# Kernel optimization log

Hardware: AMD Instinct MI355X
Metric: run time of the kernel (lower is better)

The kernel has to match this reference:

```python
import jax, jax.numpy as jnp
import numpy as np

N_TOKENS = 8192
DIM = 2048
HIDDEN = 1408
N_EXPERTS = 8
CAP = N_TOKENS // N_EXPERTS  # balanced routing: tokens per expert


def setup_inputs() -> dict:
    key = jax.random.key(0)
    kx, k1, k2, k3 = jax.random.split(key, 4)
    x = jax.random.normal(kx, (N_TOKENS, DIM), dtype=jnp.float32)
    # trunc_normal(std=0.02)-scale init approximated by scaled normal
    w1 = jax.random.normal(k1, (N_EXPERTS, HIDDEN, DIM), dtype=jnp.float32) * 0.02
    w2 = jax.random.normal(k2, (N_EXPERTS, DIM, HIDDEN), dtype=jnp.float32) * 0.02
    w3 = jax.random.normal(k3, (N_EXPERTS, HIDDEN, DIM), dtype=jnp.float32) * 0.02
    # tokens already permuted expert-contiguously; balanced load here
    num_tokens_per_expert = jnp.full((N_EXPERTS,), CAP, dtype=jnp.int32)
    return {"x": x, "num_tokens_per_expert": num_tokens_per_expert, "w1": w1, "w2": w2, "w3": w3}


def _grouped_swiglu(x, num_tokens_per_expert, w1, w2, w3):
    # x: [N, D]; w1/w3: [E, H, D]; w2: [E, D, H]. Tokens are contiguous per expert.
    E, H, D = w1.shape
    N = x.shape[0]
    cap = N // E  # fixed per-expert tile (>= max tokens of any expert here)
    offsets = jnp.cumsum(num_tokens_per_expert)
    starts = offsets - num_tokens_per_expert  # [E]

    def one_expert(w1e, w3e, w2e, start):
        # slice this expert's token tile: [cap, D]
        xe = jax.lax.dynamic_slice(x, (start, 0), (cap, D))
        h = jax.nn.silu(xe @ w1e.T) * (xe @ w3e.T)  # [cap, H] fused SwiGLU gate-up
        return h @ w2e.T  # [cap, D] down projection

    outs = jax.vmap(one_expert)(w1, w3, w2, starts)  # [E, cap, D] ragged grouped GEMM
    # mask slots beyond each expert's token count, scatter tiles back to [N, D]
    valid = jnp.arange(cap)[None, :] < num_tokens_per_expert[:, None]  # [E, cap]
    outs = jnp.where(valid[..., None], outs, jnp.zeros((), x.dtype))
    pos = jnp.clip(starts[:, None] + jnp.arange(cap)[None, :], 0, N - 1)
    out = jnp.zeros((N, D), x.dtype).at[pos.reshape(-1)].add(outs.reshape(-1, D))
    return out


def reference(x, num_tokens_per_expert, w1, w2, w3):
    return _grouped_swiglu(x, num_tokens_per_expert, w1, w2, w3)
```

## Files before the change

kernel.cpp:

```cpp
#include <hip/hip_runtime.h>
#include <hip/hip_bf16.h>

#define NT   8192
#define DD   2048
#define HH   1408
#define NE   8
#define CAPT 1024

typedef __bf16 bf16x8 __attribute__((ext_vector_type(8)));
typedef float  f32x4  __attribute__((ext_vector_type(4)));
typedef unsigned short us8 __attribute__((ext_vector_type(8)));

__device__ __forceinline__ unsigned short f2bf(float f) {
  union { float f; unsigned u; } v; v.f = f;
  unsigned r = v.u + 0x7fffu + ((v.u >> 16) & 1u);
  return (unsigned short)(r >> 16);
}

__device__ __forceinline__ void load_lds16(const void* g, void* l) {
  __builtin_amdgcn_global_load_lds(
      (const __attribute__((address_space(1))) unsigned int*)g,
      (__attribute__((address_space(3))) unsigned int*)l, 16, 0, 0);
}

__global__ __launch_bounds__(256) void cvt_bf16_kernel(
    const float* __restrict__ in, unsigned short* __restrict__ out) {
  size_t i = ((size_t)blockIdx.x * 256 + threadIdx.x) * 8;
  const float4* p = reinterpret_cast<const float4*>(in + i);
  float4 a = p[0], b = p[1];
  us8 o;
  o[0] = f2bf(a.x); o[1] = f2bf(a.y); o[2] = f2bf(a.z); o[3] = f2bf(a.w);
  o[4] = f2bf(b.x); o[5] = f2bf(b.y); o[6] = f2bf(b.z); o[7] = f2bf(b.w);
  *reinterpret_cast<us8*>(out + i) = o;
}

__global__ __launch_bounds__(256) void gateup_gemm(
    const unsigned short* __restrict__ xb,
    const unsigned short* __restrict__ w1b,
    const unsigned short* __restrict__ w3b,
    const int* __restrict__ counts,
    unsigned short* __restrict__ h)
{
  __shared__ __align__(16) unsigned short As[128 * 32];
  __shared__ __align__(16) unsigned short B1s[64 * 32];
  __shared__ __align__(16) unsigned short B3s[64 * 32];

  const int e  = blockIdx.z;
  const int m0 = blockIdx.y * 128;
  const int n0 = blockIdx.x * 64;

  int start = 0;
  for (int i = 0; i < e; ++i) start += counts[i];

  const int tid  = threadIdx.x;
  const int lane = tid & 63;
  const int wid  = tid >> 6;
  const int lrow = lane >> 2;
  const int lcol = (lane & 3) * 8;

  const unsigned short* ga  = xb  + (size_t)(start + m0 + wid * 32 + lrow) * DD + lcol;
  const unsigned short* gb1 = w1b + ((size_t)e * HH + n0 + wid * 16 + lrow) * DD + lcol;
  const unsigned short* gb3 = w3b + ((size_t)e * HH + n0 + wid * 16 + lrow) * DD + lcol;

  unsigned short* lA0 = &As [(wid * 32) * 32      + lane * 8];
  unsigned short* lA1 = &As [(wid * 32 + 16) * 32 + lane * 8];
  unsigned short* lB1 = &B1s[(wid * 16) * 32      + lane * 8];
  unsigned short* lB3 = &B3s[(wid * 16) * 32      + lane * 8];

  const int fm  = lane & 15;
  const int fko = (lane >> 4) * 8;
  const int wm  = (wid >> 1) * 64;
  const int wn  = (wid & 1) * 32;

  f32x4 acc[2][4][2] = {};

  for (int k0 = 0; k0 < DD; k0 += 32) {
    load_lds16(ga,           lA0);
    load_lds16(ga + 16 * DD, lA1);
    load_lds16(gb1,          lB1);
    load_lds16(gb3,          lB3);
    ga += 32; gb1 += 32; gb3 += 32;
    __builtin_amdgcn_s_waitcnt(0x3f70);
    __syncthreads();

    bf16x8 af[4];
#pragma unroll
    for (int i = 0; i < 4; ++i)
      af[i] = *reinterpret_cast<const bf16x8*>(&As[(wm + i * 16 + fm) * 32 + fko]);
#pragma unroll
    for (int j = 0; j < 2; ++j) {
      bf16x8 b1 = *reinterpret_cast<const bf16x8*>(&B1s[(wn + j * 16 + fm) * 32 + fko]);
      bf16x8 b3 = *reinterpret_cast<const bf16x8*>(&B3s[(wn + j * 16 + fm) * 32 + fko]);
#pragma unroll
      for (int i = 0; i < 4; ++i) {
        acc[0][i][j] = __builtin_amdgcn_mfma_f32_16x16x32_bf16(af[i], b1, acc[0][i][j], 0, 0, 0);
        acc[1][i][j] = __builtin_amdgcn_mfma_f32_16x16x32_bf16(af[i], b3, acc[1][i][j], 0, 0, 0);
      }
    }
    __syncthreads();
  }

  const int r0 = (lane >> 4) * 4;
#pragma unroll
  for (int i = 0; i < 4; ++i)
#pragma unroll
    for (int j = 0; j < 2; ++j)
#pragma unroll
      for (int r = 0; r < 4; ++r) {
        int row = m0 + wm + i * 16 + r0 + r;
        int col = n0 + wn + j * 16 + fm;
        float gv = acc[0][i][j][r];
        float uv = acc[1][i][j][r];
        float sv = (gv / (1.0f + __expf(-gv))) * uv;
        h[(size_t)(start + row) * HH + col] = f2bf(sv);
      }
}

__global__ __launch_bounds__(256) void down_gemm(
    const unsigned short* __restrict__ hb,
    const unsigned short* __restrict__ w2b,
    const int* __restrict__ counts,
    float* __restrict__ out)
{
  __shared__ __align__(16) unsigned short Hs[128 * 32];
  __shared__ __align__(16) unsigned short Ws[128 * 32];

  const int e  = blockIdx.z;
  const int m0 = blockIdx.y * 128;
  const int n0 = blockIdx.x * 128;

  int start = 0;
  for (int i = 0; i < e; ++i) start += counts[i];

  const int tid  = threadIdx.x;
  const int lane = tid & 63;
  const int wid  = tid >> 6;
  const int lrow = lane >> 2;
  const int lcol = (lane & 3) * 8;

  const unsigned short* ga = hb  + (size_t)(start + m0 + wid * 32 + lrow) * HH + lcol;
  const unsigned short* gb = w2b + ((size_t)e * DD + n0 + wid * 32 + lrow) * HH + lcol;

  unsigned short* lH0 = &Hs[(wid * 32) * 32      + lane * 8];
  unsigned short* lH1 = &Hs[(wid * 32 + 16) * 32 + lane * 8];
  unsigned short* lW0 = &Ws[(wid * 32) * 32      + lane * 8];
  unsigned short* lW1 = &Ws[(wid * 32 + 16) * 32 + lane * 8];

  const int fm  = lane & 15;
  const int fko = (lane >> 4) * 8;
  const int wm  = (wid >> 1) * 64;
  const int wn  = (wid & 1) * 64;

  f32x4 acc[4][4] = {};

  for (int k0 = 0; k0 < HH; k0 += 32) {
    load_lds16(ga,           lH0);
    load_lds16(ga + 16 * HH, lH1);
    load_lds16(gb,           lW0);
    load_lds16(gb + 16 * HH, lW1);
    ga += 32; gb += 32;
    __builtin_amdgcn_s_waitcnt(0x3f70);
    __syncthreads();

    bf16x8 af[4];
#pragma unroll
    for (int i = 0; i < 4; ++i)
      af[i] = *reinterpret_cast<const bf16x8*>(&Hs[(wm + i * 16 + fm) * 32 + fko]);
#pragma unroll
    for (int j = 0; j < 4; ++j) {
      bf16x8 bf_ = *reinterpret_cast<const bf16x8*>(&Ws[(wn + j * 16 + fm) * 32 + fko]);
#pragma unroll
      for (int i = 0; i < 4; ++i)
        acc[i][j] = __builtin_amdgcn_mfma_f32_16x16x32_bf16(af[i], bf_, acc[i][j], 0, 0, 0);
    }
    __syncthreads();
  }

  const int r0 = (lane >> 4) * 4;
#pragma unroll
  for (int i = 0; i < 4; ++i)
#pragma unroll
    for (int j = 0; j < 4; ++j)
#pragma unroll
      for (int r = 0; r < 4; ++r) {
        int row = m0 + wm + i * 16 + r0 + r;
        int col = n0 + wn + j * 16 + fm;
        out[(size_t)(start + row) * DD + col] = acc[i][j][r];
      }
}

extern "C" void kernel_launch(void* const* d_in, const int* in_sizes, int n_in,
                              void* d_out, int out_size, void* d_ws, size_t ws_size,
                              hipStream_t stream) {
  const float* x  = (const float*)d_in[0];
  const int*   cn = (const int*)d_in[1];
  const float* w1 = (const float*)d_in[2];
  const float* w2 = (const float*)d_in[3];
  const float* w3 = (const float*)d_in[4];
  float* out = (float*)d_out;

  char* ws = (char*)d_ws;
  unsigned short* xb  = (unsigned short*)(ws + 0);
  unsigned short* w1b = (unsigned short*)(ws + 33554432);
  unsigned short* w3b = (unsigned short*)(ws + 79691776);
  unsigned short* hb  = (unsigned short*)(ws + 125829120);
  unsigned short* w2b = (unsigned short*)(ws + 0);

  cvt_bf16_kernel<<<(NT * DD) / 2048, 256, 0, stream>>>(x, xb);
  cvt_bf16_kernel<<<(NE * HH * DD) / 2048, 256, 0, stream>>>(w1, w1b);
  cvt_bf16_kernel<<<(NE * HH * DD) / 2048, 256, 0, stream>>>(w3, w3b);

  dim3 g1(HH / 64, CAPT / 128, NE);
  gateup_gemm<<<g1, 256, 0, stream>>>(xb, w1b, w3b, cn, hb);

  cvt_bf16_kernel<<<(NE * DD * HH) / 2048, 256, 0, stream>>>(w2, w2b);

  dim3 g2(DD / 128, CAPT / 128, NE);
  down_gemm<<<g2, 256, 0, stream>>>(hb, w2b, cn, out);
}
```

Baseline: 533.4 us.

## Rewrite grouped GEMMs with 256-tile, double-buffered LDS pipeline and swizzled layout

Both GEMM kernels move to 512-thread blocks with 256x128 (gate-up) and 256x256 (down) tiles and a 64-wide K step. Global-to-LDS loads are double-buffered and interleaved between four MFMA phases, using explicit vmcnt waits, barriers and s_setprio. LDS uses an XOR swizzle to avoid bank conflicts, and block indices are remapped so concurrently running blocks share an expert. The aim is to raise data reuse and hide memory latency, in exchange for 128KB of dynamic LDS per block, more registers and hand-tuned synchronisation that is fragile.

```diff
diff --git a/kernel.cpp b/kernel.cpp
--- a/kernel.cpp
+++ b/kernel.cpp
@@ -1,5 +1,4 @@
 #include <hip/hip_runtime.h>
-#include <hip/hip_bf16.h>
 
 #define NT   8192
 #define DD   2048
@@ -11,6 +10,8 @@
 typedef float  f32x4  __attribute__((ext_vector_type(4)));
 typedef unsigned short us8 __attribute__((ext_vector_type(8)));
 
+#define MFMA16(a, b, c) __builtin_amdgcn_mfma_f32_16x16x32_bf16((a), (b), (c), 0, 0, 0)
+
 __device__ __forceinline__ unsigned short f2bf(float f) {
   union { float f; unsigned u; } v; v.f = f;
   unsigned r = v.u + 0x7fffu + ((v.u >> 16) & 1u);
@@ -21,6 +22,18 @@
   __builtin_amdgcn_global_load_lds(
       (const __attribute__((address_space(1))) unsigned int*)g,
       (__attribute__((address_space(3))) unsigned int*)l, 16, 0, 0);
+}
+
+#define BAR() do { asm volatile("" ::: "memory"); \
+                   __builtin_amdgcn_s_barrier();  \
+                   asm volatile("" ::: "memory"); } while (0)
+#define VMCNT6() asm volatile("s_waitcnt vmcnt(6)" ::: "memory")
+#define VMCNT0() asm volatile("s_waitcnt vmcnt(0)" ::: "memory")
+
+__device__ __forceinline__ void stage2(const unsigned short* src, unsigned short* dst,
+                                       int dchunk, int ld) {
+  load_lds16(src,                  dst + dchunk);
+  load_lds16(src + (size_t)8 * ld, dst + dchunk + 512);
 }
 
 __global__ __launch_bounds__(256) void cvt_bf16_kernel(
@@ -34,159 +47,305 @@
   *reinterpret_cast<us8*>(out + i) = o;
 }
 
-__global__ __launch_bounds__(256) void gateup_gemm(
+__global__ __launch_bounds__(512, 2) void gateup_gemm(
     const unsigned short* __restrict__ xb,
     const unsigned short* __restrict__ w1b,
     const unsigned short* __restrict__ w3b,
     const int* __restrict__ counts,
     unsigned short* __restrict__ h)
 {
-  __shared__ __align__(16) unsigned short As[128 * 32];
-  __shared__ __align__(16) unsigned short B1s[64 * 32];
-  __shared__ __align__(16) unsigned short B3s[64 * 32];
-
-  const int e  = blockIdx.z;
-  const int m0 = blockIdx.y * 128;
-  const int n0 = blockIdx.x * 64;
+  extern __shared__ unsigned short lds[];
+
+  int lin = blockIdx.x + 11 * (blockIdx.y + 4 * blockIdx.z);
+  lin = (lin & 7) * 44 + (lin >> 3);
+  const int e   = lin / 44;
+  const int rem = lin - e * 44;
+  const int m0  = (rem / 11) * 256;
+  const int n0  = (rem - (rem / 11) * 11) * 128;
 
   int start = 0;
   for (int i = 0; i < e; ++i) start += counts[i];
 
   const int tid  = threadIdx.x;
   const int lane = tid & 63;
-  const int wid  = tid >> 6;
-  const int lrow = lane >> 2;
-  const int lcol = (lane & 3) * 8;
-
-  const unsigned short* ga  = xb  + (size_t)(start + m0 + wid * 32 + lrow) * DD + lcol;
-  const unsigned short* gb1 = w1b + ((size_t)e * HH + n0 + wid * 16 + lrow) * DD + lcol;
-  const unsigned short* gb3 = w3b + ((size_t)e * HH + n0 + wid * 16 + lrow) * DD + lcol;
-
-  unsigned short* lA0 = &As [(wid * 32) * 32      + lane * 8];
-  unsigned short* lA1 = &As [(wid * 32 + 16) * 32 + lane * 8];
-  unsigned short* lB1 = &B1s[(wid * 16) * 32      + lane * 8];
-  unsigned short* lB3 = &B3s[(wid * 16) * 32      + lane * 8];
-
-  const int fm  = lane & 15;
-  const int fko = (lane >> 4) * 8;
-  const int wm  = (wid >> 1) * 64;
-  const int wn  = (wid & 1) * 32;
-
-  f32x4 acc[2][4][2] = {};
-
-  for (int k0 = 0; k0 < DD; k0 += 32) {
-    load_lds16(ga,           lA0);
-    load_lds16(ga + 16 * DD, lA1);
-    load_lds16(gb1,          lB1);
-    load_lds16(gb3,          lB3);
-    ga += 32; gb1 += 32; gb3 += 32;
-    __builtin_amdgcn_s_waitcnt(0x3f70);
-    __syncthreads();
-
-    bf16x8 af[4];
-#pragma unroll
-    for (int i = 0; i < 4; ++i)
-      af[i] = *reinterpret_cast<const bf16x8*>(&As[(wm + i * 16 + fm) * 32 + fko]);
-#pragma unroll
-    for (int j = 0; j < 2; ++j) {
-      bf16x8 b1 = *reinterpret_cast<const bf16x8*>(&B1s[(wn + j * 16 + fm) * 32 + fko]);
-      bf16x8 b3 = *reinterpret_cast<const bf16x8*>(&B3s[(wn + j * 16 + fm) * 32 + fko]);
-#pragma unroll
-      for (int i = 0; i < 4; ++i) {
-        acc[0][i][j] = __builtin_amdgcn_mfma_f32_16x16x32_bf16(af[i], b1, acc[0][i][j], 0, 0, 0);
-        acc[1][i][j] = __builtin_amdgcn_mfma_f32_16x16x32_bf16(af[i], b3, acc[1][i][j], 0, 0, 0);
-      }
-    }
-    __syncthreads();
+  const int w    = tid >> 6;
+  const int wr   = w >> 2;
+  const int wc   = w & 3;
+  const int fm   = lane & 15;
+  const int l4   = lane >> 4;
+  const int s0   = (l4 ^ (fm & 7)) << 3;
+  const int s1   = s0 ^ 32;
+  const int srcR = w * 16 + (lane >> 3);
+  const int srcC = ((lane & 7) ^ (lane >> 3)) << 3;
+  const int dchunk = w * 1024 + lane * 8;
+
+  const unsigned short* gA  = xb  + (size_t)(start + m0 + srcR) * DD + srcC;
+  const unsigned short* gB1 = w1b + ((size_t)e * HH + n0 + srcR) * DD + srcC;
+  const unsigned short* gB3 = w3b + ((size_t)e * HH + n0 + srcR) * DD + srcC;
+
+  unsigned short* ldsA = lds;
+  unsigned short* ldsB = lds + 32768;
+
+  stage2(gA,                       ldsA,                 dchunk, DD);
+  stage2(gA + (size_t)128 * DD,    ldsA + 8192,          dchunk, DD);
+  stage2(gB1,                      ldsB,                 dchunk, DD);
+  stage2(gB3,                      ldsB + 8192,          dchunk, DD);
+  stage2(gB1 + 64,                 ldsB + 16384,         dchunk, DD);
+  stage2(gA + 64,                  ldsA + 16384,         dchunk, DD);
+  stage2(gA + (size_t)128 * DD + 64, ldsA + 16384 + 8192, dchunk, DD);
+  VMCNT6();
+  BAR();
+
+  f32x4 accG[8][2] = {};
+  f32x4 accU[8][2] = {};
+  const int NTL = DD / 64;
+
+  for (int t = 0; t < NTL; ++t) {
+    const int buf  = (t & 1) << 14;
+    const int obuf = buf ^ 16384;
+    const unsigned short* At = ldsA + buf + wr * 8192 + fm * 64;
+    const unsigned short* Bg = ldsB + buf + (wc * 32 + fm) * 64;
+    const unsigned short* Bu = Bg + 8192;
+    bf16x8 a0[4][2], a1[4][2], bg[2][2], bu[2][2];
+
+#pragma unroll
+    for (int mi = 0; mi < 4; ++mi) {
+      a0[mi][0] = *(const bf16x8*)(At + mi * 1024 + s0);
+      a0[mi][1] = *(const bf16x8*)(At + mi * 1024 + s1);
+    }
+#pragma unroll
+    for (int nj = 0; nj < 2; ++nj) {
+      bg[nj][0] = *(const bf16x8*)(Bg + nj * 1024 + s0);
+      bg[nj][1] = *(const bf16x8*)(Bg + nj * 1024 + s1);
+    }
+    if (t + 1 < NTL) stage2(gB3 + (t + 1) * 64, ldsB + obuf + 8192, dchunk, DD);
+    BAR();
+    __builtin_amdgcn_s_setprio(1);
+#pragma unroll
+    for (int mi = 0; mi < 4; ++mi)
+#pragma unroll
+      for (int nj = 0; nj < 2; ++nj) {
+        accG[mi][nj] = MFMA16(a0[mi][0], bg[nj][0], accG[mi][nj]);
+        accG[mi][nj] = MFMA16(a0[mi][1], bg[nj][1], accG[mi][nj]);
+      }
+    __builtin_amdgcn_s_setprio(0);
+    BAR();
+
+#pragma unroll
+    for (int mi = 0; mi < 4; ++mi) {
+      a1[mi][0] = *(const bf16x8*)(At + (mi + 4) * 1024 + s0);
+      a1[mi][1] = *(const bf16x8*)(At + (mi + 4) * 1024 + s1);
+    }
+    if (t + 2 < NTL) stage2(gB1 + (t + 2) * 64, ldsB + buf, dchunk, DD);
+    BAR();
+    __builtin_amdgcn_s_setprio(1);
+#pragma unroll
+    for (int mi = 0; mi < 4; ++mi)
+#pragma unroll
+      for (int nj = 0; nj < 2; ++nj) {
+        accG[mi + 4][nj] = MFMA16(a1[mi][0], bg[nj][0], accG[mi + 4][nj]);
+        accG[mi + 4][nj] = MFMA16(a1[mi][1], bg[nj][1], accG[mi + 4][nj]);
+      }
+    __builtin_amdgcn_s_setprio(0);
+    BAR();
+
+#pragma unroll
+    for (int nj = 0; nj < 2; ++nj) {
+      bu[nj][0] = *(const bf16x8*)(Bu + nj * 1024 + s0);
+      bu[nj][1] = *(const bf16x8*)(Bu + nj * 1024 + s1);
+    }
+    if (t + 2 < NTL) stage2(gA + (t + 2) * 64, ldsA + buf, dchunk, DD);
+    BAR();
+    __builtin_amdgcn_s_setprio(1);
+#pragma unroll
+    for (int mi = 0; mi < 4; ++mi)
+#pragma unroll
+      for (int nj = 0; nj < 2; ++nj) {
+        accU[mi][nj] = MFMA16(a0[mi][0], bu[nj][0], accU[mi][nj]);
+        accU[mi][nj] = MFMA16(a0[mi][1], bu[nj][1], accU[mi][nj]);
+      }
+    __builtin_amdgcn_s_setprio(0);
+    BAR();
+
+    if (t + 2 < NTL) {
+      stage2(gA + (size_t)128 * DD + (t + 2) * 64, ldsA + buf + 8192, dchunk, DD);
+      VMCNT6();
+    } else if (t + 1 < NTL) {
+      VMCNT0();
+    }
+    BAR();
+    __builtin_amdgcn_s_setprio(1);
+#pragma unroll
+    for (int mi = 0; mi < 4; ++mi)
+#pragma unroll
+      for (int nj = 0; nj < 2; ++nj) {
+        accU[mi + 4][nj] = MFMA16(a1[mi][0], bu[nj][0], accU[mi + 4][nj]);
+        accU[mi + 4][nj] = MFMA16(a1[mi][1], bu[nj][1], accU[mi + 4][nj]);
+      }
+    __builtin_amdgcn_s_setprio(0);
+    BAR();
   }
 
-  const int r0 = (lane >> 4) * 4;
-#pragma unroll
-  for (int i = 0; i < 4; ++i)
-#pragma unroll
-    for (int j = 0; j < 2; ++j)
+  const int r0 = l4 * 4;
+  const size_t hbase = (size_t)(start + m0 + wr * 128) * HH + n0 + wc * 32 + fm;
+#pragma unroll
+  for (int mi = 0; mi < 8; ++mi)
+#pragma unroll
+    for (int nj = 0; nj < 2; ++nj)
 #pragma unroll
       for (int r = 0; r < 4; ++r) {
-        int row = m0 + wm + i * 16 + r0 + r;
-        int col = n0 + wn + j * 16 + fm;
-        float gv = acc[0][i][j][r];
-        float uv = acc[1][i][j][r];
+        float gv = accG[mi][nj][r];
+        float uv = accU[mi][nj][r];
         float sv = (gv / (1.0f + __expf(-gv))) * uv;
-        h[(size_t)(start + row) * HH + col] = f2bf(sv);
-      }
-}
-
-__global__ __launch_bounds__(256) void down_gemm(
+        h[hbase + (size_t)(mi * 16 + r0 + r) * HH + nj * 16] = f2bf(sv);
+      }
+}
+
+__global__ __launch_bounds__(512, 2) void down_gemm(
     const unsigned short* __restrict__ hb,
     const unsigned short* __restrict__ w2b,
     const int* __restrict__ counts,
     float* __restrict__ out)
 {
-  __shared__ __align__(16) unsigned short Hs[128 * 32];
-  __shared__ __align__(16) unsigned short Ws[128 * 32];
-
-  const int e  = blockIdx.z;
-  const int m0 = blockIdx.y * 128;
-  const int n0 = blockIdx.x * 128;
+  extern __shared__ unsigned short lds[];
+
+  int lin = blockIdx.x + 8 * (blockIdx.y + 4 * blockIdx.z);
+  lin = (lin & 7) * 32 + (lin >> 3);
+  const int e   = lin >> 5;
+  const int rem = lin & 31;
+  const int m0  = (rem >> 3) * 256;
+  const int n0  = (rem & 7) * 256;
 
   int start = 0;
   for (int i = 0; i < e; ++i) start += counts[i];
 
   const int tid  = threadIdx.x;
   const int lane = tid & 63;
-  const int wid  = tid >> 6;
-  const int lrow = lane >> 2;
-  const int lcol = (lane & 3) * 8;
-
-  const unsigned short* ga = hb  + (size_t)(start + m0 + wid * 32 + lrow) * HH + lcol;
-  const unsigned short* gb = w2b + ((size_t)e * DD + n0 + wid * 32 + lrow) * HH + lcol;
-
-  unsigned short* lH0 = &Hs[(wid * 32) * 32      + lane * 8];
-  unsigned short* lH1 = &Hs[(wid * 32 + 16) * 32 + lane * 8];
-  unsigned short* lW0 = &Ws[(wid * 32) * 32      + lane * 8];
-  unsigned short* lW1 = &Ws[(wid * 32 + 16) * 32 + lane * 8];
-
-  const int fm  = lane & 15;
-  const int fko = (lane >> 4) * 8;
-  const int wm  = (wid >> 1) * 64;
-  const int wn  = (wid & 1) * 64;
-
-  f32x4 acc[4][4] = {};
-
-  for (int k0 = 0; k0 < HH; k0 += 32) {
-    load_lds16(ga,           lH0);
-    load_lds16(ga + 16 * HH, lH1);
-    load_lds16(gb,           lW0);
-    load_lds16(gb + 16 * HH, lW1);
-    ga += 32; gb += 32;
-    __builtin_amdgcn_s_waitcnt(0x3f70);
-    __syncthreads();
-
-    bf16x8 af[4];
-#pragma unroll
-    for (int i = 0; i < 4; ++i)
-      af[i] = *reinterpret_cast<const bf16x8*>(&Hs[(wm + i * 16 + fm) * 32 + fko]);
-#pragma unroll
-    for (int j = 0; j < 4; ++j) {
-      bf16x8 bf_ = *reinterpret_cast<const bf16x8*>(&Ws[(wn + j * 16 + fm) * 32 + fko]);
-#pragma unroll
-      for (int i = 0; i < 4; ++i)
-        acc[i][j] = __builtin_amdgcn_mfma_f32_16x16x32_bf16(af[i], bf_, acc[i][j], 0, 0, 0);
-    }
-    __syncthreads();
+  const int w    = tid >> 6;
+  const int wr   = w >> 2;
+  const int wc   = w & 3;
+  const int fm   = lane & 15;
+  const int l4   = lane >> 4;
+  const int s0   = (l4 ^ (fm & 7)) << 3;
+  const int s1   = s0 ^ 32;
+  const int srcR = w * 16 + (lane >> 3);
+  const int srcC = ((lane & 7) ^ (lane >> 3)) << 3;
+  const int dchunk = w * 1024 + lane * 8;
+
+  const unsigned short* gA = hb  + (size_t)(start + m0 + srcR) * HH + srcC;
+  const unsigned short* gB = w2b + ((size_t)e * DD + n0 + srcR) * HH + srcC;
+
+  unsigned short* ldsA = lds;
+  unsigned short* ldsB = lds + 32768;
+
+  stage2(gA,                       ldsA,                 dchunk, HH);
+  stage2(gA + (size_t)128 * HH,    ldsA + 8192,          dchunk, HH);
+  stage2(gB,                       ldsB,                 dchunk, HH);
+  stage2(gB + (size_t)128 * HH,    ldsB + 8192,          dchunk, HH);
+  stage2(gA + 64,                  ldsA + 16384,         dchunk, HH);
+  stage2(gA + (size_t)128 * HH + 64, ldsA + 16384 + 8192, dchunk, HH);
+  stage2(gB + 64,                  ldsB + 16384,         dchunk, HH);
+  VMCNT6();
+  BAR();
+
+  f32x4 acc[8][4] = {};
+  const int NTL = HH / 64;
+
+  for (int t = 0; t < NTL; ++t) {
+    const int buf  = (t & 1) << 14;
+    const int obuf = buf ^ 16384;
+    const unsigned short* At = ldsA + buf + wr * 8192 + fm * 64;
+    const unsigned short* Bt = ldsB + buf + (wc >> 1) * 8192 + ((wc & 1) * 64 + fm) * 64;
+    bf16x8 a0[4][2], a1[4][2], b0[2][2], b1[2][2];
+
+#pragma unroll
+    for (int mi = 0; mi < 4; ++mi) {
+      a0[mi][0] = *(const bf16x8*)(At + mi * 1024 + s0);
+      a0[mi][1] = *(const bf16x8*)(At + mi * 1024 + s1);
+    }
+#pragma unroll
+    for (int nj = 0; nj < 2; ++nj) {
+      b0[nj][0] = *(const bf16x8*)(Bt + nj * 1024 + s0);
+      b0[nj][1] = *(const bf16x8*)(Bt + nj * 1024 + s1);
+    }
+    if (t + 1 < NTL)
+      stage2(gB + (size_t)128 * HH + (t + 1) * 64, ldsB + obuf + 8192, dchunk, HH);
+    BAR();
+    __builtin_amdgcn_s_setprio(1);
+#pragma unroll
+    for (int mi = 0; mi < 4; ++mi)
+#pragma unroll
+      for (int nj = 0; nj < 2; ++nj) {
+        acc[mi][nj] = MFMA16(a0[mi][0], b0[nj][0], acc[mi][nj]);
+        acc[mi][nj] = MFMA16(a0[mi][1], b0[nj][1], acc[mi][nj]);
+      }
+    __builtin_amdgcn_s_setprio(0);
+    BAR();
+
+#pragma unroll
+    for (int mi = 0; mi < 4; ++mi) {
+      a1[mi][0] = *(const bf16x8*)(At + (mi + 4) * 1024 + s0);
+      a1[mi][1] = *(const bf16x8*)(At + (mi + 4) * 1024 + s1);
+    }
+    BAR();
+    __builtin_amdgcn_s_setprio(1);
+#pragma unroll
+    for (int mi = 0; mi < 4; ++mi)
+#pragma unroll
+      for (int nj = 0; nj < 2; ++nj) {
+        acc[mi + 4][nj] = MFMA16(a1[mi][0], b0[nj][0], acc[mi + 4][nj]);
+        acc[mi + 4][nj] = MFMA16(a1[mi][1], b0[nj][1], acc[mi + 4][nj]);
+      }
+    __builtin_amdgcn_s_setprio(0);
+    BAR();
+
+#pragma unroll
+    for (int nj = 0; nj < 2; ++nj) {
+      b1[nj][0] = *(const bf16x8*)(Bt + (nj + 2) * 1024 + s0);
+      b1[nj][1] = *(const bf16x8*)(Bt + (nj + 2) * 1024 + s1);
+    }
+    if (t + 2 < NTL) stage2(gA + (t + 2) * 64, ldsA + buf, dchunk, HH);
+    BAR();
+    __builtin_amdgcn_s_setprio(1);
+#pragma unroll
+    for (int mi = 0; mi < 4; ++mi)
+#pragma unroll
+      for (int nj = 0; nj < 2; ++nj) {
+        acc[mi][nj + 2] = MFMA16(a0[mi][0], b1[nj][0], acc[mi][nj + 2]);
+        acc[mi][nj + 2] = MFMA16(a0[mi][1], b1[nj][1], acc[mi][nj + 2]);
+      }
+    __builtin_amdgcn_s_setprio(0);
+    BAR();
+
+    if (t + 2 < NTL) {
+      stage2(gA + (size_t)128 * HH + (t + 2) * 64, ldsA + buf + 8192, dchunk, HH);
+      stage2(gB + (t + 2) * 64,                    ldsB + buf,        dchunk, HH);
+      VMCNT6();
+    } else if (t + 1 < NTL) {
+      VMCNT0();
+    }
+    BAR();
+    __builtin_amdgcn_s_setprio(1);
+#pragma unroll
+    for (int mi = 0; mi < 4; ++mi)
+#pragma unroll
+      for (int nj = 0; nj < 2; ++nj) {
+        acc[mi + 4][nj + 2] = MFMA16(a1[mi][0], b1[nj][0], acc[mi + 4][nj + 2]);
+        acc[mi + 4][nj + 2] = MFMA16(a1[mi][1], b1[nj][1], acc[mi + 4][nj + 2]);
+      }
+    __builtin_amdgcn_s_setprio(0);
+    BAR();
   }
 
-  const int r0 = (lane >> 4) * 4;
-#pragma unroll
-  for (int i = 0; i < 4; ++i)
-#pragma unroll
-    for (int j = 0; j < 4; ++j)
-#pragma unroll
-      for (int r = 0; r < 4; ++r) {
-        int row = m0 + wm + i * 16 + r0 + r;
-        int col = n0 + wn + j * 16 + fm;
-        out[(size_t)(start + row) * DD + col] = acc[i][j][r];
-      }
+  const int r0 = l4 * 4;
+  const size_t obase = (size_t)(start + m0 + wr * 128) * DD + n0 + wc * 64 + fm;
+#pragma unroll
+  for (int mi = 0; mi < 8; ++mi)
+#pragma unroll
+    for (int nj = 0; nj < 4; ++nj)
+#pragma unroll
+      for (int r = 0; r < 4; ++r)
+        out[obase + (size_t)(mi * 16 + r0 + r) * DD + nj * 16] = acc[mi][nj][r];
 }
 
 extern "C" void kernel_launch(void* const* d_in, const int* in_sizes, int n_in,
@@ -206,15 +365,24 @@
   unsigned short* hb  = (unsigned short*)(ws + 125829120);
   unsigned short* w2b = (unsigned short*)(ws + 0);
 
+  static int attr_set = 0;
+  if (!attr_set) {
+    (void)hipFuncSetAttribute((const void*)gateup_gemm,
+                              hipFuncAttributeMaxDynamicSharedMemorySize, 131072);
+    (void)hipFuncSetAttribute((const void*)down_gemm,
+                              hipFuncAttributeMaxDynamicSharedMemorySize, 131072);
+    attr_set = 1;
+  }
+
   cvt_bf16_kernel<<<(NT * DD) / 2048, 256, 0, stream>>>(x, xb);
   cvt_bf16_kernel<<<(NE * HH * DD) / 2048, 256, 0, stream>>>(w1, w1b);
   cvt_bf16_kernel<<<(NE * HH * DD) / 2048, 256, 0, stream>>>(w3, w3b);
 
-  dim3 g1(HH / 64, CAPT / 128, NE);
-  gateup_gemm<<<g1, 256, 0, stream>>>(xb, w1b, w3b, cn, hb);
+  dim3 g1(HH / 128, CAPT / 256, NE);
+  gateup_gemm<<<g1, 512, 131072, stream>>>(xb, w1b, w3b, cn, hb);
 
   cvt_bf16_kernel<<<(NE * DD * HH) / 2048, 256, 0, stream>>>(w2, w2b);
 
-  dim3 g2(DD / 128, CAPT / 128, NE);
-  down_gemm<<<g2, 256, 0, stream>>>(hb, w2b, cn, out);
-}
+  dim3 g2(DD / 256, CAPT / 256, NE);
+  down_gemm<<<g2, 512, 131072, stream>>>(hb, w2b, cn, out);
+}
```

New measurement: 476.6 us. 1.12x faster.
